# Kernel tuning notes

Measured on AMD Instinct MI355X. Metric: run time of the kernel, lower is better.

Reference implementation:

```python
import jax, jax.numpy as jnp
import numpy as np
from jax import lax

B, E, D, N, R, K = 4, 768, 1536, 16, 48, 4
H, W = 16, 16
L = H * W
NDIR = 4


def _perms():
    idx = np.arange(L)
    idx_v = np.arange(L).reshape(H, W).T.reshape(-1)  # column-major (vertical) scan order
    perms = [idx, idx[::-1].copy(), idx_v, idx_v[::-1].copy()]
    invs = [np.argsort(p) for p in perms]
    return [jnp.asarray(p) for p in perms], [jnp.asarray(p) for p in invs]

PERMS, INVS = _perms()


def setup_inputs() -> dict:
    key = jax.random.key(0)
    ks = jax.random.split(key, 10)
    hidden_states = jax.random.normal(ks[0], (B, L, E), jnp.float32)
    in_proj_w = jax.random.normal(ks[1], (2 * D, E), jnp.float32) * 0.02
    out_proj_w = jax.random.normal(ks[2], (E, D), jnp.float32) * 0.02
    conv_w = jax.random.normal(ks[3], (NDIR, D, K), jnp.float32) * 0.1
    conv_b = jax.random.normal(ks[4], (NDIR, D), jnp.float32) * 0.1
    xproj_w = jax.random.normal(ks[5], (NDIR, R + 2 * N, D), jnp.float32) * 0.02
    dt_init_std = R ** -0.5
    dtproj_w = jax.random.uniform(ks[6], (NDIR, D, R), jnp.float32, -dt_init_std, dt_init_std)
    dt = jnp.exp(jax.random.uniform(ks[7], (NDIR, D), jnp.float32)
                 * (np.log(0.1) - np.log(0.001)) + np.log(0.001))
    dt = jnp.clip(dt, 1e-4, None)
    dtproj_b = dt + jnp.log(-jnp.expm1(-dt))  # inverse-softplus init as in the module
    A_log = jnp.broadcast_to(
        jnp.log(jnp.arange(1, N + 1, dtype=jnp.float32))[None, None, :], (NDIR, D, N)).copy()
    D_param = jnp.ones((NDIR, D), jnp.float32)
    return dict(hidden_states=hidden_states, in_proj_w=in_proj_w, out_proj_w=out_proj_w,
                conv_w=conv_w, conv_b=conv_b, xproj_w=xproj_w, dtproj_w=dtproj_w,
                dtproj_b=dtproj_b, A_log=A_log, D_param=D_param)


def _mamba_dir(xz, cw, cb, xw, dtw, dtb, a_log, dpar):
    # xz: (B, 2D, L) in this direction's scan order
    x, z = xz[:, :D], xz[:, D:]
    # causal depthwise conv1d + SiLU (mamba_inner_fn conv path)
    x = lax.conv_general_dilated(x, cw[:, None, :], (1,), [(K - 1, 0)],
                                 feature_group_count=D,
                                 dimension_numbers=('NCH', 'OIH', 'NCH'))
    x = jax.nn.silu(x + cb[None, :, None])
    # x_proj -> dt, B, C
    x_dbl = jnp.einsum('bdl,kd->bkl', x, xw)
    dt, Bm, Cm = x_dbl[:, :R], x_dbl[:, R:R + N], x_dbl[:, R + N:]
    delta = jax.nn.softplus(jnp.einsum('brl,dr->bdl', dt, dtw) + dtb[None, :, None])
    A = -jnp.exp(a_log)                                  # (D, N)
    dA = jnp.exp(jnp.einsum('bdl,dn->lbdn', delta, A))   # (L, B, D, N)
    dBu = jnp.einsum('bdl,bnl,bdl->lbdn', delta, Bm, x)  # delta * B * u

    def step(h, inp):
        da, dbu = inp
        h = da * h + dbu
        return h, h

    h0 = jnp.zeros((x.shape[0], D, N), x.dtype)
    _, hs = lax.scan(step, h0, (dA, dBu))                # (L, B, D, N)
    y = jnp.einsum('lbdn,bnl->bdl', hs, Cm) + dpar[None, :, None] * x
    return y * jax.nn.silu(z)                            # gate, (B, D, L)


def reference(hidden_states, in_proj_w, out_proj_w, conv_w, conv_b,
              xproj_w, dtproj_w, dtproj_b, A_log, D_param):
    xz = jnp.einsum('ble,fe->bfl', hidden_states, in_proj_w)  # (B, 2D, L)
    out = jnp.zeros((hidden_states.shape[0], D, L), hidden_states.dtype)
    for i in range(NDIR):  # fixed small set of structurally distinct scan directions
        xz_i = xz[:, :, PERMS[i]]
        y = _mamba_dir(xz_i, conv_w[i], conv_b[i], xproj_w[i], dtproj_w[i],
                       dtproj_b[i], A_log[i], D_param[i])
        out = out + y[:, :, INVS[i]]  # multi_reverse then sum-fusion
    return jnp.einsum('bdl,ed->ble', out, out_proj_w)
```

## Files before the change

### kernel.cpp

```cpp
#include <hip/hip_runtime.h>
#include <hip/hip_bf16.h>

#define BI   4
#define LI   256
#define EI   768
#define DI   1536
#define NI   16
#define RI   48
#define KI   4
#define NDIRS 4
#define F2D  3072
#define MROWS 1024
#define LOG2E 1.4426950408889634f

typedef float    floatx2 __attribute__((ext_vector_type(2)));
typedef float    floatx4 __attribute__((ext_vector_type(4)));
typedef _Float16 halfx2  __attribute__((ext_vector_type(2)));
typedef _Float16 halfx4  __attribute__((ext_vector_type(4)));
typedef _Float16 halfx8  __attribute__((ext_vector_type(8)));

typedef __attribute__((address_space(3))) unsigned lds_u32;
typedef __attribute__((address_space(1))) const unsigned glb_u32;

__device__ __forceinline__ void load16(const _Float16* g, _Float16* l) {
    __builtin_amdgcn_global_load_lds((glb_u32*)g, (lds_u32*)l, 16, 0, 0);
}

__device__ __forceinline__ int perm_idx(int dir, int j) {
    switch (dir) {
        case 0:  return j;
        case 1:  return 255 - j;
        case 2:  return ((j & 15) << 4) | (j >> 4);
        default: return 255 - (((j & 15) << 4) | (j >> 4));
    }
}

template<int CTRL>
__device__ __forceinline__ float dpp_add(float p) {
    int t = __builtin_amdgcn_update_dpp(0, __builtin_bit_cast(int, p),
                                        CTRL, 0xf, 0xf, true);
    return p + __builtin_bit_cast(float, t);
}
__device__ __forceinline__ float grp8_sum(float p) {
    p = dpp_add<0xB1>(p);
    p = dpp_add<0x4E>(p);
    p = dpp_add<0x141>(p);
    return p;
}

template<int BM, int BN, int WGN, int FM, int FN>
__device__ __forceinline__ void gemm_core(const _Float16* __restrict__ Ah,
                                          const _Float16* __restrict__ Al, int lda,
                                          const _Float16* __restrict__ Bh,
                                          const _Float16* __restrict__ Bl, int ldb,
                                          int nChunks, _Float16* smem,
                                          floatx4 (&acc)[FM][FN]) {
    const int tid = threadIdx.x, lane = tid & 63, wave = tid >> 6;
    const int wave_m = wave / WGN, wave_n = wave % WGN;
    _Float16* sAh = smem;
    _Float16* sAl = smem + BM * 32;
    _Float16* sBh = smem + BM * 64;
    _Float16* sBl = smem + BM * 64 + BN * 32;
    const int rr = lane & 15, koff = (lane >> 4) * 8;
    const int arow = wave_m * FM * 16, brow = wave_n * FN * 16;

    for (int c = 0; c < nChunks; ++c) {
        for (int idx = tid; idx < BM * 4; idx += 256) {
            int r = idx >> 2, s = (idx & 3) * 8;
            load16(Ah + (size_t)r * lda + c * 32 + s, sAh + idx * 8);
            load16(Al + (size_t)r * lda + c * 32 + s, sAl + idx * 8);
        }
        for (int idx = tid; idx < BN * 4; idx += 256) {
            int r = idx >> 2, s = (idx & 3) * 8;
            load16(Bh + (size_t)r * ldb + c * 32 + s, sBh + idx * 8);
            load16(Bl + (size_t)r * ldb + c * 32 + s, sBl + idx * 8);
        }
        asm volatile("s_waitcnt vmcnt(0)" ::: "memory");
        __syncthreads();

        halfx8 ahf[FM], alf[FM], bhf[FN], blf[FN];
        #pragma unroll
        for (int i = 0; i < FM; ++i) {
            ahf[i] = *(const halfx8*)(sAh + (arow + i * 16 + rr) * 32 + koff);
            alf[i] = *(const halfx8*)(sAl + (arow + i * 16 + rr) * 32 + koff);
        }
        #pragma unroll
        for (int j = 0; j < FN; ++j) {
            bhf[j] = *(const halfx8*)(sBh + (brow + j * 16 + rr) * 32 + koff);
            blf[j] = *(const halfx8*)(sBl + (brow + j * 16 + rr) * 32 + koff);
        }
        #pragma unroll
        for (int i = 0; i < FM; ++i)
            #pragma unroll
            for (int j = 0; j < FN; ++j) {
                acc[i][j] = __builtin_amdgcn_mfma_f32_16x16x32_f16(ahf[i], bhf[j], acc[i][j], 0, 0, 0);
                acc[i][j] = __builtin_amdgcn_mfma_f32_16x16x32_f16(ahf[i], blf[j], acc[i][j], 0, 0, 0);
                acc[i][j] = __builtin_amdgcn_mfma_f32_16x16x32_f16(alf[i], bhf[j], acc[i][j], 0, 0, 0);
            }
        __syncthreads();
    }
}

__global__ __launch_bounds__(256) void k_splitall(
        const float* __restrict__ hs,  const float* __restrict__ wip,
        const float* __restrict__ wop, const float* __restrict__ xw,
        const float* __restrict__ dtw,
        _Float16* __restrict__ hsh,  _Float16* __restrict__ hsl,
        _Float16* __restrict__ wiph, _Float16* __restrict__ wipl,
        _Float16* __restrict__ woph, _Float16* __restrict__ wopl,
        _Float16* __restrict__ xwh,  _Float16* __restrict__ xwl,
        _Float16* __restrict__ dtwh, _Float16* __restrict__ dtwl) {
    int i4 = (blockIdx.x * 256 + threadIdx.x) * 4;
    floatx4 v;
    _Float16 *dh, *dl; int off;
    if (i4 < 786432)        { off = i4;           v = *(const floatx4*)(hs + off);  dh = hsh;  dl = hsl;  }
    else if (i4 < 3145728)  { off = i4 - 786432;  v = *(const floatx4*)(wip + off); dh = wiph; dl = wipl; }
    else if (i4 < 4325376)  { off = i4 - 3145728; v = *(const floatx4*)(wop + off); dh = woph; dl = wopl; }
    else if (i4 < 4816896)  { off = i4 - 4325376; v = *(const floatx4*)(xw + off);  dh = xwh;  dl = xwl;  }
    else {
        int t0 = i4 - 4816896;
        int col = t0 & 63, dr = t0 >> 6;
        floatx4 z = {0.f, 0.f, 0.f, 0.f};
        v = (col < 48) ? *(const floatx4*)(dtw + (size_t)dr * 48 + col) : z;
        dh = dtwh; dl = dtwl; off = t0;
    }
    halfx4 hh, hl;
    #pragma unroll
    for (int e = 0; e < 4; ++e) {
        _Float16 h = (_Float16)v[e];
        hh[e] = h; hl[e] = (_Float16)(v[e] - (float)h);
    }
    *(halfx4*)(dh + off) = hh;
    *(halfx4*)(dl + off) = hl;
}

__global__ __launch_bounds__(256) void k_inproj_t(const _Float16* __restrict__ Ah,
                                                  const _Float16* __restrict__ Al,
                                                  const _Float16* __restrict__ Bh,
                                                  const _Float16* __restrict__ Bl,
                                                  float* __restrict__ C) {
    __shared__ _Float16 smem[128 * 64 + 128 * 64];
    int row0 = blockIdx.x * 128, col0 = blockIdx.y * 128, k0 = blockIdx.z * 384;
    float* Cp = C + (size_t)blockIdx.z * MROWS * F2D;
    floatx4 acc[4][4] = {};
    gemm_core<128, 128, 2, 4, 4>(Ah + (size_t)row0 * EI + k0, Al + (size_t)row0 * EI + k0, EI,
                                 Bh + (size_t)col0 * EI + k0, Bl + (size_t)col0 * EI + k0, EI,
                                 12, smem, acc);
    int lane = threadIdx.x & 63, wave = threadIdx.x >> 6;
    int cc = lane & 15, q = lane >> 4;
    int rbase = row0 + (wave >> 1) * 64, cbase = col0 + (wave & 1) * 64;
    #pragma unroll
    for (int i = 0; i < 4; ++i)
        #pragma unroll
        for (int j = 0; j < 4; ++j)
            #pragma unroll
            for (int r = 0; r < 4; ++r)
                Cp[(size_t)(rbase + i * 16 + q * 4 + r) * F2D + cbase + j * 16 + cc] = acc[i][j][r];
}

__global__ __launch_bounds__(256) void k_outproj_t(const _Float16* __restrict__ Ah,
                                                   const _Float16* __restrict__ Al,
                                                   const _Float16* __restrict__ Bh,
                                                   const _Float16* __restrict__ Bl,
                                                   float* __restrict__ C) {
    __shared__ _Float16 smem[192 * 64];
    int row0 = blockIdx.x * 64, col0 = blockIdx.y * 128, k0 = blockIdx.z * 384;
    float* Cp = C + (size_t)blockIdx.z * MROWS * EI;
    floatx4 acc[2][4] = {};
    gemm_core<64, 128, 2, 2, 4>(Ah + (size_t)row0 * DI + k0, Al + (size_t)row0 * DI + k0, DI,
                                Bh + (size_t)col0 * DI + k0, Bl + (size_t)col0 * DI + k0, DI,
                                12, smem, acc);
    int lane = threadIdx.x & 63, wave = threadIdx.x >> 6;
    int cc = lane & 15, q = lane >> 4;
    int rbase = row0 + (wave >> 1) * 32, cbase = col0 + (wave & 1) * 64;
    #pragma unroll
    for (int i = 0; i < 2; ++i)
        #pragma unroll
        for (int j = 0; j < 4; ++j)
            #pragma unroll
            for (int r = 0; r < 4; ++r)
                Cp[(size_t)(rbase + i * 16 + q * 4 + r) * EI + cbase + j * 16 + cc] = acc[i][j][r];
}

__global__ __launch_bounds__(256) void k_osum(const float* __restrict__ oacc,
                                              float* __restrict__ out) {
    int i4 = (blockIdx.x * 256 + threadIdx.x) * 4;
    const size_t S = (size_t)MROWS * EI;
    floatx4 s = *(const floatx4*)(oacc + i4) + *(const floatx4*)(oacc + S + i4) +
                *(const floatx4*)(oacc + 2 * S + i4) + *(const floatx4*)(oacc + 3 * S + i4);
    *(floatx4*)(out + i4) = s;
}

__global__ __launch_bounds__(256) void k_xdbl_t(const _Float16* __restrict__ xh,
                                                const _Float16* __restrict__ xl,
                                                const _Float16* __restrict__ xwh,
                                                const _Float16* __restrict__ xwl,
                                                float* __restrict__ C) {
    __shared__ _Float16 smem[208 * 64];
    int row0 = blockIdx.x * 128, dir = blockIdx.y, k0 = blockIdx.z * 192;
    float* Cp = C + (size_t)blockIdx.z * NDIRS * MROWS * 80;
    floatx4 acc[2][5] = {};
    const size_t abase = ((size_t)dir * MROWS + row0) * DI + k0;
    const size_t bbase = (size_t)dir * 80 * DI + k0;
    gemm_core<128, 80, 1, 2, 5>(xh + abase, xl + abase, DI,
                                xwh + bbase, xwl + bbase, DI, 6, smem, acc);
    int lane = threadIdx.x & 63, wave = threadIdx.x >> 6;
    int cc = lane & 15, q = lane >> 4;
    int rbase = row0 + wave * 32;
    #pragma unroll
    for (int i = 0; i < 2; ++i)
        #pragma unroll
        for (int j = 0; j < 5; ++j)
            #pragma unroll
            for (int r = 0; r < 4; ++r)
                Cp[((size_t)dir * MROWS + rbase + i * 16 + q * 4 + r) * 80 + j * 16 + cc] = acc[i][j][r];
}

__global__ __launch_bounds__(256) void k_xsplit(const float* __restrict__ acc,
                                                _Float16* __restrict__ dtqh,
                                                _Float16* __restrict__ dtql,
                                                float* __restrict__ BCm) {
    const size_t PS = (size_t)NDIRS * MROWS * 80;
    int idx = blockIdx.x * 256 + threadIdx.x;
    int dir = idx / (MROWS * 96);
    int rem = idx - dir * MROWS * 96;
    int row = rem / 96, col = rem - row * 96;
    size_t rbase = (size_t)dir * MROWS + row;
    auto sum8 = [&](int c) {
        size_t o = rbase * 80 + c;
        float s = 0.f;
        #pragma unroll
        for (int kp = 0; kp < 8; ++kp) s += acc[kp * PS + o];
        return s;
    };
    if (col < 64) {
        float v = (col < 48) ? sum8(col) : 0.f;
        _Float16 h = (_Float16)v;
        dtqh[rbase * 64 + col] = h;
        dtql[rbase * 64 + col] = (_Float16)(v - (float)h);
    } else if (col < 80) {
        int n = col - 64;
        BCm[rbase * 32 + n * 2] = sum8(48 + n);
    } else {
        int n = col - 80;
        BCm[rbase * 32 + n * 2 + 1] = sum8(64 + n);
    }
}

__global__ __launch_bounds__(256) void k_delta_t(const _Float16* __restrict__ dtqh,
                                                 const _Float16* __restrict__ dtql,
                                                 const _Float16* __restrict__ dtwh,
                                                 const _Float16* __restrict__ dtwl,
                                                 const float* __restrict__ dtb,
                                                 float* __restrict__ delta) {
    __shared__ _Float16 smem[192 * 64];
    int row0 = blockIdx.x * 64, col0 = blockIdx.y * 128, dir = blockIdx.z;
    floatx4 acc[2][4] = {};
    const size_t abase = ((size_t)dir * MROWS + row0) * 64;
    const size_t bbase = ((size_t)dir * DI + col0) * 64;
    gemm_core<64, 128, 2, 2, 4>(dtqh + abase, dtql + abase, 64,
                                dtwh + bbase, dtwl + bbase, 64, 2, smem, acc);
    int lane = threadIdx.x & 63, wave = threadIdx.x >> 6;
    int cc = lane & 15, q = lane >> 4;
    int rbase = row0 + (wave >> 1) * 32, cbase = col0 + (wave & 1) * 64;
    #pragma unroll
    for (int i = 0; i < 2; ++i)
        #pragma unroll
        for (int j = 0; j < 4; ++j) {
            int col = cbase + j * 16 + cc;
            float bias = dtb[(size_t)dir * DI + col];
            #pragma unroll
            for (int r = 0; r < 4; ++r) {
                float v = acc[i][j][r] + bias;
                float sp = (v > 20.f) ? v : log1pf(__expf(v));
                delta[((size_t)dir * MROWS + rbase + i * 16 + q * 4 + r) * DI + col] = sp;
            }
        }
}

__global__ __launch_bounds__(256) void k_conv(const float* __restrict__ xz,
                                              const float* __restrict__ cw,
                                              const float* __restrict__ cb,
                                              _Float16* __restrict__ xh,
                                              _Float16* __restrict__ xl) {
    const size_t S = (size_t)MROWS * F2D;
    int dir = blockIdx.z, b = blockIdx.y;
    int lchunk = blockIdx.x / 6, dsub = blockIdx.x % 6;
    int d = dsub * 256 + threadIdx.x;
    int base = lchunk * 16;

    const float* w = cw + ((size_t)dir * DI + d) * KI;
    float w0 = w[0], w1 = w[1], w2 = w[2], w3 = w[3];
    float bias = cb[(size_t)dir * DI + d];

    auto ld = [&](int m) -> float {
        if (m < 0) return 0.f;
        int src = perm_idx(dir, m);
        size_t o = ((size_t)b * 256 + src) * F2D + d;
        return xz[o] + xz[S + o];
    };
    float xm3 = ld(base - 3), xm2 = ld(base - 2), xm1 = ld(base - 1);

    #pragma unroll
    for (int j = 0; j < 16; ++j) {
        float cur = ld(base + j);
        float s = bias + w0 * xm3 + w1 * xm2 + w2 * xm1 + w3 * cur;
        xm3 = xm2; xm2 = xm1; xm1 = cur;
        float x = s / (1.f + __expf(-s));
        _Float16 h = (_Float16)x;
        size_t o = ((size_t)dir * MROWS + b * 256 + base + j) * DI + d;
        xh[o] = h;
        xl[o] = (_Float16)(x - (float)h);
    }
}

__global__ __launch_bounds__(256) void k_scan(const float* __restrict__ delta,
                                              const _Float16* __restrict__ xhg,
                                              const _Float16* __restrict__ xlg,
                                              const float* __restrict__ xz,
                                              const float* __restrict__ BCm,
                                              const float* __restrict__ A_log,
                                              const float* __restrict__ Dp,
                                              float* __restrict__ ydir) {
    const size_t S = (size_t)MROWS * F2D;
    const int dchunk = blockIdx.x, b = blockIdx.y, dir = blockIdx.z;
    const int tid = threadIdx.x;
    const int dslot = tid >> 3;
    const int np = tid & 7;
    const int d0 = dchunk * 32, d = d0 + dslot;

    __shared__ float sdx[2][32][64];
    __shared__ float sbc[2][32][32];
    __shared__ float sY[32][32];

    const float Av0 = -__expf(A_log[((size_t)dir * DI + d) * NI + 2 * np]) * LOG2E;
    const float Av1 = -__expf(A_log[((size_t)dir * DI + d) * NI + 2 * np + 1]) * LOG2E;
    const float Dpar = Dp[(size_t)dir * DI + d];
    float h0 = 0.f, h1 = 0.f;

    const size_t dirrow = (size_t)dir * MROWS;
    const int srow = tid >> 3, sc4 = (tid & 7) * 4;

    floatx4 rdel, rbc, rz;
    halfx4 rxh, rxl;
    auto load_chunk = [&](int j0) {
        int row = b * 256 + j0 + srow;
        size_t o = (dirrow + row) * DI + d0 + sc4;
        rdel = *(const floatx4*)(delta + o);
        rxh  = *(const halfx4*)(xhg + o);
        rxl  = *(const halfx4*)(xlg + o);
        rbc  = *(const floatx4*)(BCm + (dirrow + row) * 32 + sc4);
        int lsrc = perm_idx(dir, j0 + srow);
        size_t zo = ((size_t)b * 256 + lsrc) * F2D + DI + d0 + sc4;
        floatx4 z0 = *(const floatx4*)(xz + zo);
        floatx4 z1 = *(const floatx4*)(xz + S + zo);
        rz = z0 + z1;
    };

    load_chunk(0);

    for (int c = 0; c < 8; ++c) {
        const int buf = c & 1;
        #pragma unroll
        for (int e = 0; e < 4; ++e) {
            sdx[buf][srow][(sc4 + e) * 2]     = rdel[e];
            sdx[buf][srow][(sc4 + e) * 2 + 1] = (float)rxh[e] + (float)rxl[e];
        }
        *(floatx4*)&sbc[buf][srow][sc4] = rbc;
        floatx4 zs = rz;
        __syncthreads();
        if (c < 7) load_chunk((c + 1) * 32);

        #pragma unroll
        for (int jj = 0; jj < 32; ++jj) {
            floatx2 dx = *(const floatx2*)&sdx[buf][jj][dslot * 2];
            floatx4 bc = *(const floatx4*)&sbc[buf][jj][np * 4];
            float dv = dx[0], xv = dx[1];
            float a0 = __builtin_amdgcn_exp2f(dv * Av0);
            float a1 = __builtin_amdgcn_exp2f(dv * Av1);
            float du = dv * xv;
            h0 = fmaf(a0, h0, du * bc[0]);
            h1 = fmaf(a1, h1, du * bc[2]);
            float p = fmaf(h1, bc[3], h0 * bc[1]);
            p = grp8_sum(p);
            if (np == 0) sY[jj][dslot] = fmaf(Dpar, xv, p);
        }
        __syncthreads();

        {
            int lout = perm_idx(dir, c * 32 + srow);
            floatx4 o;
            #pragma unroll
            for (int e = 0; e < 4; ++e) {
                float zv = zs[e];
                float g = zv / (1.f + __expf(-zv));
                o[e] = sY[srow][sc4 + e] * g;
            }
            *(floatx4*)&ydir[(dirrow + (size_t)b * 256 + lout) * DI + d0 + sc4] = o;
        }
    }
}

__global__ __launch_bounds__(256) void k_sum(const float* __restrict__ ydir,
                                             _Float16* __restrict__ yh,
                                             _Float16* __restrict__ yl) {
    int i4 = (blockIdx.x * 256 + threadIdx.x) * 4;
    const size_t S = (size_t)MROWS * DI;
    floatx4 s = *(const floatx4*)(ydir + i4) + *(const floatx4*)(ydir + S + i4) +
                *(const floatx4*)(ydir + 2 * S + i4) + *(const floatx4*)(ydir + 3 * S + i4);
    halfx4 hh, hl;
    #pragma unroll
    for (int e = 0; e < 4; ++e) {
        _Float16 h = (_Float16)s[e];
        hh[e] = h; hl[e] = (_Float16)(s[e] - (float)h);
    }
    *(halfx4*)(yh + i4) = hh;
    *(halfx4*)(yl + i4) = hl;
}

extern "C" void kernel_launch(void* const* d_in, const int* in_sizes, int n_in,
                              void* d_out, int out_size, void* d_ws, size_t ws_size,
                              hipStream_t stream) {
    const float* hs   = (const float*)d_in[0];
    const float* wip  = (const float*)d_in[1];
    const float* wop  = (const float*)d_in[2];
    const float* cw   = (const float*)d_in[3];
    const float* cb   = (const float*)d_in[4];
    const float* xw   = (const float*)d_in[5];
    const float* dtw  = (const float*)d_in[6];
    const float* dtb  = (const float*)d_in[7];
    const float* alog = (const float*)d_in[8];
    const float* dpar = (const float*)d_in[9];
    float* out = (float*)d_out;

    char* p = (char*)d_ws;
    auto alloc_f32 = [&](size_t n) { float* r = (float*)p; p += n * 4; return r; };
    auto alloc_f16 = [&](size_t n) { _Float16* r = (_Float16*)p; p += n * 2; return r; };

    _Float16* hsh  = alloc_f16(786432);
    _Float16* hsl  = alloc_f16(786432);
    _Float16* wiph = alloc_f16(2359296);
    _Float16* wipl = alloc_f16(2359296);
    _Float16* woph = alloc_f16(1179648);
    _Float16* wopl = alloc_f16(1179648);
    _Float16* xwh  = alloc_f16(491520);
    _Float16* xwl  = alloc_f16(491520);
    _Float16* dtwh = alloc_f16((size_t)NDIRS * DI * 64);
    _Float16* dtwl = alloc_f16((size_t)NDIRS * DI * 64);
    float*    xz   = alloc_f32((size_t)2 * MROWS * F2D);
    _Float16* xh   = alloc_f16((size_t)NDIRS * MROWS * DI);
    _Float16* xl   = alloc_f16((size_t)NDIRS * MROWS * DI);
    _Float16* dtqh = alloc_f16((size_t)NDIRS * MROWS * 64);
    _Float16* dtql = alloc_f16((size_t)NDIRS * MROWS * 64);
    float*    BCm  = alloc_f32((size_t)NDIRS * MROWS * 32);
    float*    delta= alloc_f32((size_t)NDIRS * MROWS * DI);
    float*    ydir = alloc_f32((size_t)NDIRS * MROWS * DI);
    _Float16* yh   = alloc_f16((size_t)MROWS * DI);
    _Float16* yl   = alloc_f16((size_t)MROWS * DI);

    float* xdba = ydir;
    float* oacc = delta;

    k_splitall<<<dim3(5088), 256, 0, stream>>>(hs, wip, wop, xw, dtw,
                                               hsh, hsl, wiph, wipl, woph, wopl,
                                               xwh, xwl, dtwh, dtwl);
    k_inproj_t<<<dim3(8, 24, 2), 256, 0, stream>>>(hsh, hsl, wiph, wipl, xz);
    k_conv    <<<dim3(96, BI, NDIRS), 256, 0, stream>>>(xz, cw, cb, xh, xl);
    k_xdbl_t  <<<dim3(8, NDIRS, 8), 256, 0, stream>>>(xh, xl, xwh, xwl, xdba);
    k_xsplit  <<<dim3(1536), 256, 0, stream>>>(xdba, dtqh, dtql, BCm);
    k_delta_t <<<dim3(16, 12, NDIRS), 256, 0, stream>>>(dtqh, dtql, dtwh, dtwl, dtb, delta);
    k_scan    <<<dim3(DI / 32, BI, NDIRS), 256, 0, stream>>>(delta, xh, xl, xz, BCm,
                                                             alog, dpar, ydir);
    k_sum     <<<dim3(1536), 256, 0, stream>>>(ydir, yh, yl);
    k_outproj_t<<<dim3(16, 6, 4), 256, 0, stream>>>(yh, yl, woph, wopl, oacc);
    k_osum    <<<dim3(768), 256, 0, stream>>>(oacc, out);
}
```

Baseline: 235.0 us.

## Split selective scan into chunked three-pass parallel scan and move gating into sum

The sequential 256-step scan per block is replaced by three passes. Each of 8 sequence chunks first computes its local state and decay product, a small kernel then carries prefix states across chunks, and a third pass reruns each chunk from its carried-in state to produce outputs. This gives 8x more blocks to hide the serial recurrence latency, at the cost of doing the exp/FMA scan work roughly twice plus extra global traffic for the chunk states. The SiLU(z) gate is the same for every direction at a given position, so it is factored out of the per-direction scan and applied once in the summation kernel.

```diff
diff --git a/kernel.cpp b/kernel.cpp
--- a/kernel.cpp
+++ b/kernel.cpp
@@ -12,6 +12,8 @@
 #define F2D  3072
 #define MROWS 1024
 #define LOG2E 1.4426950408889634f
+#define NCH  8
+#define PLANE (NDIRS * BI * DI * NI)
 
 typedef float    floatx2 __attribute__((ext_vector_type(2)));
 typedef float    floatx4 __attribute__((ext_vector_type(4)));
@@ -314,105 +316,159 @@
     }
 }
 
-__global__ __launch_bounds__(256) void k_scan(const float* __restrict__ delta,
-                                              const _Float16* __restrict__ xhg,
-                                              const _Float16* __restrict__ xlg,
-                                              const float* __restrict__ xz,
-                                              const float* __restrict__ BCm,
-                                              const float* __restrict__ A_log,
-                                              const float* __restrict__ Dp,
-                                              float* __restrict__ ydir) {
-    const size_t S = (size_t)MROWS * F2D;
-    const int dchunk = blockIdx.x, b = blockIdx.y, dir = blockIdx.z;
+__global__ __launch_bounds__(256) void k_scanA(const float* __restrict__ delta,
+                                               const _Float16* __restrict__ xhg,
+                                               const _Float16* __restrict__ xlg,
+                                               const float* __restrict__ BCm,
+                                               const float* __restrict__ A_log,
+                                               float* __restrict__ Pb,
+                                               float* __restrict__ Sb) {
+    const int dchunk = blockIdx.x, b = blockIdx.y;
+    const int dir = blockIdx.z >> 3, lc = blockIdx.z & 7;
     const int tid = threadIdx.x;
-    const int dslot = tid >> 3;
-    const int np = tid & 7;
+    const int dslot = tid >> 3, np = tid & 7;
     const int d0 = dchunk * 32, d = d0 + dslot;
 
-    __shared__ float sdx[2][32][64];
-    __shared__ float sbc[2][32][32];
+    __shared__ float sdx[32][64];
+    __shared__ float sbc[32][32];
+
+    const float Av0 = -__expf(A_log[((size_t)dir * DI + d) * NI + 2 * np]) * LOG2E;
+    const float Av1 = -__expf(A_log[((size_t)dir * DI + d) * NI + 2 * np + 1]) * LOG2E;
+
+    const size_t dirrow = (size_t)dir * MROWS;
+    const int srow = tid >> 3, sc4 = (tid & 7) * 4;
+    {
+        int row = b * 256 + lc * 32 + srow;
+        size_t o = (dirrow + row) * DI + d0 + sc4;
+        floatx4 rdel = *(const floatx4*)(delta + o);
+        halfx4 rxh = *(const halfx4*)(xhg + o);
+        halfx4 rxl = *(const halfx4*)(xlg + o);
+        floatx4 rbc = *(const floatx4*)(BCm + (dirrow + row) * 32 + sc4);
+        #pragma unroll
+        for (int e = 0; e < 4; ++e) {
+            sdx[srow][(sc4 + e) * 2]     = rdel[e];
+            sdx[srow][(sc4 + e) * 2 + 1] = (float)rxh[e] + (float)rxl[e];
+        }
+        *(floatx4*)&sbc[srow][sc4] = rbc;
+    }
+    __syncthreads();
+
+    float h0 = 0.f, h1 = 0.f, P0 = 1.f, P1 = 1.f;
+    #pragma unroll
+    for (int jj = 0; jj < 32; ++jj) {
+        floatx2 dx = *(const floatx2*)&sdx[jj][dslot * 2];
+        floatx4 bc = *(const floatx4*)&sbc[jj][np * 4];
+        float dv = dx[0], xv = dx[1];
+        float a0 = __builtin_amdgcn_exp2f(dv * Av0);
+        float a1 = __builtin_amdgcn_exp2f(dv * Av1);
+        float du = dv * xv;
+        h0 = fmaf(a0, h0, du * bc[0]);
+        h1 = fmaf(a1, h1, du * bc[2]);
+        P0 *= a0; P1 *= a1;
+    }
+    size_t i0 = ((size_t)(dir * BI + b) * DI + d) * NI + 2 * np;
+    floatx2 pv = {P0, P1}, sv = {h0, h1};
+    *(floatx2*)(Pb + (size_t)lc * PLANE + i0) = pv;
+    *(floatx2*)(Sb + (size_t)lc * PLANE + i0) = sv;
+}
+
+__global__ __launch_bounds__(256) void k_scanB(const float* __restrict__ Pb,
+                                               const float* __restrict__ Sb,
+                                               float* __restrict__ Hs) {
+    int i = blockIdx.x * 256 + threadIdx.x;
+    float h = 0.f;
+    #pragma unroll
+    for (int c = 0; c < NCH; ++c) {
+        Hs[(size_t)c * PLANE + i] = h;
+        h = fmaf(Pb[(size_t)c * PLANE + i], h, Sb[(size_t)c * PLANE + i]);
+    }
+}
+
+__global__ __launch_bounds__(256) void k_scanC(const float* __restrict__ delta,
+                                               const _Float16* __restrict__ xhg,
+                                               const _Float16* __restrict__ xlg,
+                                               const float* __restrict__ BCm,
+                                               const float* __restrict__ A_log,
+                                               const float* __restrict__ Dp,
+                                               const float* __restrict__ Hs,
+                                               float* __restrict__ ydir) {
+    const int dchunk = blockIdx.x, b = blockIdx.y;
+    const int dir = blockIdx.z >> 3, lc = blockIdx.z & 7;
+    const int tid = threadIdx.x;
+    const int dslot = tid >> 3, np = tid & 7;
+    const int d0 = dchunk * 32, d = d0 + dslot;
+
+    __shared__ float sdx[32][64];
+    __shared__ float sbc[32][32];
     __shared__ float sY[32][32];
 
     const float Av0 = -__expf(A_log[((size_t)dir * DI + d) * NI + 2 * np]) * LOG2E;
     const float Av1 = -__expf(A_log[((size_t)dir * DI + d) * NI + 2 * np + 1]) * LOG2E;
     const float Dpar = Dp[(size_t)dir * DI + d];
-    float h0 = 0.f, h1 = 0.f;
 
     const size_t dirrow = (size_t)dir * MROWS;
     const int srow = tid >> 3, sc4 = (tid & 7) * 4;
-
-    floatx4 rdel, rbc, rz;
-    halfx4 rxh, rxl;
-    auto load_chunk = [&](int j0) {
-        int row = b * 256 + j0 + srow;
+    {
+        int row = b * 256 + lc * 32 + srow;
         size_t o = (dirrow + row) * DI + d0 + sc4;
-        rdel = *(const floatx4*)(delta + o);
-        rxh  = *(const halfx4*)(xhg + o);
-        rxl  = *(const halfx4*)(xlg + o);
-        rbc  = *(const floatx4*)(BCm + (dirrow + row) * 32 + sc4);
-        int lsrc = perm_idx(dir, j0 + srow);
-        size_t zo = ((size_t)b * 256 + lsrc) * F2D + DI + d0 + sc4;
-        floatx4 z0 = *(const floatx4*)(xz + zo);
-        floatx4 z1 = *(const floatx4*)(xz + S + zo);
-        rz = z0 + z1;
-    };
-
-    load_chunk(0);
-
-    for (int c = 0; c < 8; ++c) {
-        const int buf = c & 1;
+        floatx4 rdel = *(const floatx4*)(delta + o);
+        halfx4 rxh = *(const halfx4*)(xhg + o);
+        halfx4 rxl = *(const halfx4*)(xlg + o);
+        floatx4 rbc = *(const floatx4*)(BCm + (dirrow + row) * 32 + sc4);
         #pragma unroll
         for (int e = 0; e < 4; ++e) {
-            sdx[buf][srow][(sc4 + e) * 2]     = rdel[e];
-            sdx[buf][srow][(sc4 + e) * 2 + 1] = (float)rxh[e] + (float)rxl[e];
-        }
-        *(floatx4*)&sbc[buf][srow][sc4] = rbc;
-        floatx4 zs = rz;
-        __syncthreads();
-        if (c < 7) load_chunk((c + 1) * 32);
-
-        #pragma unroll
-        for (int jj = 0; jj < 32; ++jj) {
-            floatx2 dx = *(const floatx2*)&sdx[buf][jj][dslot * 2];
-            floatx4 bc = *(const floatx4*)&sbc[buf][jj][np * 4];
-            float dv = dx[0], xv = dx[1];
-            float a0 = __builtin_amdgcn_exp2f(dv * Av0);
-            float a1 = __builtin_amdgcn_exp2f(dv * Av1);
-            float du = dv * xv;
-            h0 = fmaf(a0, h0, du * bc[0]);
-            h1 = fmaf(a1, h1, du * bc[2]);
-            float p = fmaf(h1, bc[3], h0 * bc[1]);
-            p = grp8_sum(p);
-            if (np == 0) sY[jj][dslot] = fmaf(Dpar, xv, p);
-        }
-        __syncthreads();
-
-        {
-            int lout = perm_idx(dir, c * 32 + srow);
-            floatx4 o;
-            #pragma unroll
-            for (int e = 0; e < 4; ++e) {
-                float zv = zs[e];
-                float g = zv / (1.f + __expf(-zv));
-                o[e] = sY[srow][sc4 + e] * g;
-            }
-            *(floatx4*)&ydir[(dirrow + (size_t)b * 256 + lout) * DI + d0 + sc4] = o;
-        }
+            sdx[srow][(sc4 + e) * 2]     = rdel[e];
+            sdx[srow][(sc4 + e) * 2 + 1] = (float)rxh[e] + (float)rxl[e];
+        }
+        *(floatx4*)&sbc[srow][sc4] = rbc;
+    }
+    size_t i0 = ((size_t)(dir * BI + b) * DI + d) * NI + 2 * np;
+    floatx2 hv = *(const floatx2*)(Hs + (size_t)lc * PLANE + i0);
+    float h0 = hv[0], h1 = hv[1];
+    __syncthreads();
+
+    #pragma unroll
+    for (int jj = 0; jj < 32; ++jj) {
+        floatx2 dx = *(const floatx2*)&sdx[jj][dslot * 2];
+        floatx4 bc = *(const floatx4*)&sbc[jj][np * 4];
+        float dv = dx[0], xv = dx[1];
+        float a0 = __builtin_amdgcn_exp2f(dv * Av0);
+        float a1 = __builtin_amdgcn_exp2f(dv * Av1);
+        float du = dv * xv;
+        h0 = fmaf(a0, h0, du * bc[0]);
+        h1 = fmaf(a1, h1, du * bc[2]);
+        float p = fmaf(h1, bc[3], h0 * bc[1]);
+        p = grp8_sum(p);
+        if (np == 0) sY[jj][dslot] = fmaf(Dpar, xv, p);
+    }
+    __syncthreads();
+
+    {
+        int lout = perm_idx(dir, lc * 32 + srow);
+        floatx4 o = *(const floatx4*)&sY[srow][sc4];
+        *(floatx4*)&ydir[(dirrow + (size_t)b * 256 + lout) * DI + d0 + sc4] = o;
     }
 }
 
 __global__ __launch_bounds__(256) void k_sum(const float* __restrict__ ydir,
+                                             const float* __restrict__ xz,
                                              _Float16* __restrict__ yh,
                                              _Float16* __restrict__ yl) {
     int i4 = (blockIdx.x * 256 + threadIdx.x) * 4;
     const size_t S = (size_t)MROWS * DI;
+    const size_t SZ = (size_t)MROWS * F2D;
+    int row = i4 / DI, dcol = i4 - row * DI;
+    size_t zo = (size_t)row * F2D + DI + dcol;
+    floatx4 zv = *(const floatx4*)(xz + zo) + *(const floatx4*)(xz + SZ + zo);
     floatx4 s = *(const floatx4*)(ydir + i4) + *(const floatx4*)(ydir + S + i4) +
                 *(const floatx4*)(ydir + 2 * S + i4) + *(const floatx4*)(ydir + 3 * S + i4);
     halfx4 hh, hl;
     #pragma unroll
     for (int e = 0; e < 4; ++e) {
-        _Float16 h = (_Float16)s[e];
-        hh[e] = h; hl[e] = (_Float16)(s[e] - (float)h);
+        float g = zv[e] / (1.f + __expf(-zv[e]));
+        float v = s[e] * g;
+        _Float16 h = (_Float16)v;
+        hh[e] = h; hl[e] = (_Float16)(v - (float)h);
     }
     *(halfx4*)(yh + i4) = hh;
     *(halfx4*)(yl + i4) = hl;
@@ -459,6 +515,9 @@
     _Float16* yl   = alloc_f16((size_t)MROWS * DI);
 
     float* xdba = ydir;
+    float* Pb   = ydir;
+    float* Sb   = ydir + (size_t)NCH * PLANE;
+    float* Hst  = (float*)d_ws;
     float* oacc = delta;
 
     k_splitall<<<dim3(5088), 256, 0, stream>>>(hs, wip, wop, xw, dtw,
@@ -469,9 +528,11 @@
     k_xdbl_t  <<<dim3(8, NDIRS, 8), 256, 0, stream>>>(xh, xl, xwh, xwl, xdba);
     k_xsplit  <<<dim3(1536), 256, 0, stream>>>(xdba, dtqh, dtql, BCm);
     k_delta_t <<<dim3(16, 12, NDIRS), 256, 0, stream>>>(dtqh, dtql, dtwh, dtwl, dtb, delta);
-    k_scan    <<<dim3(DI / 32, BI, NDIRS), 256, 0, stream>>>(delta, xh, xl, xz, BCm,
-                                                             alog, dpar, ydir);
-    k_sum     <<<dim3(1536), 256, 0, stream>>>(ydir, yh, yl);
+    k_scanA   <<<dim3(48, BI, NDIRS * NCH), 256, 0, stream>>>(delta, xh, xl, BCm, alog, Pb, Sb);
+    k_scanB   <<<dim3(PLANE / 256), 256, 0, stream>>>(Pb, Sb, Hst);
+    k_scanC   <<<dim3(48, BI, NDIRS * NCH), 256, 0, stream>>>(delta, xh, xl, BCm, alog, dpar,
+                                                              Hst, ydir);
+    k_sum     <<<dim3(1536), 256, 0, stream>>>(ydir, xz, yh, yl);
     k_outproj_t<<<dim3(16, 6, 4), 256, 0, stream>>>(yh, yl, woph, wopl, oacc);
     k_osum    <<<dim3(768), 256, 0, stream>>>(oacc, out);
 }
```

Result: slower. 252.0 us (+7.2%).
